# Performance work log

Measured on AMD Instinct MI355X. Metric: run time of the kernel, lower is better.

Reference implementation:

```python
import jax, jax.numpy as jnp
import numpy as np

B, T, H = 2, 2048, 1024
NH = 16
HD = H // NH


def setup_inputs() -> dict:
    key = jax.random.key(0)
    ks = jax.random.split(key, 9)
    s = 0.02
    return {
        "x": jax.random.normal(ks[0], (B, T, H), dtype=jnp.float32),
        "attn_mask": jnp.ones((B, T), dtype=jnp.int32),
        "Wq": jax.random.normal(ks[1], (H, H), dtype=jnp.float32) * s,
        "bq": jnp.zeros((H,), dtype=jnp.float32),
        "Wk": jax.random.normal(ks[2], (H, H), dtype=jnp.float32) * s,
        "bk": jnp.zeros((H,), dtype=jnp.float32),
        "Wv": jax.random.normal(ks[3], (H, H), dtype=jnp.float32) * s,
        "bv": jnp.zeros((H,), dtype=jnp.float32),
        "Wo": jax.random.normal(ks[4], (H, H), dtype=jnp.float32) * s,
        "bo": jnp.zeros((H,), dtype=jnp.float32),
    }


def reference(x, attn_mask, Wq, bq, Wk, bk, Wv, bv, Wo, bo):
    Bc, Tc, Hc = x.shape
    scale = HD ** -0.5
    # projections; torch Linear: y = x @ W.T + b (here W stored as [in,out])
    q = (x @ Wq + bq).reshape(Bc, Tc, NH, HD).transpose(0, 2, 1, 3)  # [B,NH,T,HD]
    k = (x @ Wk + bk).reshape(Bc, Tc, NH, HD).transpose(0, 2, 1, 3)
    v = (x @ Wv + bv).reshape(Bc, Tc, NH, HD).transpose(0, 2, 1, 3)
    scores = jnp.einsum('bhqd,bhkd->bhqk', q, k) * scale  # [B,NH,T,T]
    mask = attn_mask.reshape(Bc, 1, 1, Tc)
    scores = jnp.where(mask == 0, jnp.float32(-jnp.inf), scores)
    probs = jax.nn.softmax(scores, axis=-1)
    ctx = jnp.einsum('bhqk,bhkd->bhqd', probs, v)  # [B,NH,T,HD]
    ctx = ctx.transpose(0, 2, 1, 3).reshape(Bc, Tc, Hc)
    out = ctx @ Wo + bo
    return out
```

## Files before the change

### kernel.cpp

```cpp
#include <hip/hip_runtime.h>

typedef _Float16 f16;
typedef _Float16 f16x8 __attribute__((ext_vector_type(8)));
typedef _Float16 f16x4 __attribute__((ext_vector_type(4)));
typedef __fp16 h16x2 __attribute__((ext_vector_type(2)));
typedef float f32x4 __attribute__((ext_vector_type(4)));

#define MFMA32(a, b, c) __builtin_amdgcn_mfma_f32_16x16x32_f16((a), (b), (c), 0, 0, 0)
#define MFMA16(a, b, c) __builtin_amdgcn_mfma_f32_16x16x16f16((a), (b), (c), 0, 0, 0)

static constexpr int Bb = 2, T = 2048, H = 1024, NH = 16, HD = 64;
static constexpr int M = Bb * T;
static constexpr int NQKV = 3 * H;
#define QSCALE 0.1803368801111f

__device__ __forceinline__ void gload_lds16(const void* g, void* l) {
  __builtin_amdgcn_global_load_lds(
      (const __attribute__((address_space(1))) void*)g,
      (__attribute__((address_space(3))) void*)l, 16, 0, 0);
}


__global__ __launch_bounds__(256) void cvt_f32_f16_x4(const float* __restrict__ in,
                                                      f16* __restrict__ out, int n4) {
  int i = blockIdx.x * 256 + threadIdx.x;
  if (i < n4) {
    float4 v = ((const float4*)in)[i];
    f16x4 o;
    o[0] = (f16)v.x; o[1] = (f16)v.y; o[2] = (f16)v.z; o[3] = (f16)v.w;
    *(f16x4*)(out + (size_t)i * 4) = o;
  }
}

__global__ __launch_bounds__(256) void transpose_cvt4(const float* __restrict__ Wq,
                                                      const float* __restrict__ Wk,
                                                      const float* __restrict__ Wv,
                                                      const float* __restrict__ Wo,
                                                      f16* __restrict__ WqkvT,
                                                      f16* __restrict__ WoT) {
  const int z = blockIdx.z;
  const float* W = (z == 0) ? Wq : (z == 1) ? Wk : (z == 2) ? Wv : Wo;
  f16* Wt = (z < 3) ? (WqkvT + (size_t)z * H * H) : WoT;
  const float scale = (z == 0) ? QSCALE : 1.0f;
  __shared__ f16 tile[64][65];
  int k0 = blockIdx.y * 64, n0 = blockIdx.x * 64;
  for (int p = 0; p < 16; ++p) {
    int idx = threadIdx.x + p * 256;
    int r = idx >> 6, c = idx & 63;
    tile[r][c] = (f16)(W[(size_t)(k0 + r) * H + n0 + c] * scale);
  }
  __syncthreads();
  for (int p = 0; p < 16; ++p) {
    int idx = threadIdx.x + p * 256;
    int r = idx >> 6, c = idx & 63;
    Wt[(size_t)(n0 + r) * H + k0 + c] = tile[c][r];
  }
}

__global__ void pack_bias(const float* __restrict__ bq, const float* __restrict__ bk,
                          const float* __restrict__ bv, float* __restrict__ o) {
  int i = blockIdx.x * 256 + threadIdx.x;
  if (i < 3072) {
    float v = (i < 1024) ? bq[i] * QSCALE : ((i < 2048) ? bk[i - 1024] : bv[i - 2048]);
    o[i] = v;
  }
}

__device__ __forceinline__ f16x8 lds_frag(const f16* base, int row, int gr) {
  return *(const f16x8*)(base + row * 64 + ((gr ^ (row & 7)) << 3));
}

template <int TM, int TN, bool OUT_F32>
__global__ __launch_bounds__(256) void gemm_f16_bt(const f16* __restrict__ A,
                                                   const f16* __restrict__ Bt,
                                                   const float* __restrict__ bias,
                                                   void* __restrict__ Cout,
                                                   int Nn, int Kk) {
  __shared__ f16 As[TM * 64];
  __shared__ f16 Bs[TN * 64];
  const int tid = threadIdx.x;
  const int lane = tid & 63, w = tid >> 6;
  const int quad = lane >> 4, l16 = lane & 15;
  const int wm = w >> 1, wn = w & 1;
  const int m0 = blockIdx.y * TM, n0 = blockIdx.x * TN;
  constexpr int AM = TM / 32, AN = TN / 32;

  f32x4 acc[AM][AN];
  for (int a = 0; a < AM; ++a)
    for (int b2 = 0; b2 < AN; ++b2)
      for (int r = 0; r < 4; ++r) acc[a][b2][r] = 0.f;

  for (int k0 = 0; k0 < Kk; k0 += 64) {
    for (int p = 0; p < TM * 8 / 256; ++p) {
      int slot = p * 256 + w * 64 + lane;
      int r = slot >> 3, g = (slot & 7) ^ (r & 7);
      gload_lds16(A + (size_t)(m0 + r) * Kk + k0 + g * 8,
                  (char*)As + (p * 256 + w * 64) * 16);
    }
    for (int p = 0; p < TN * 8 / 256; ++p) {
      int slot = p * 256 + w * 64 + lane;
      int r = slot >> 3, g = (slot & 7) ^ (r & 7);
      gload_lds16(Bt + (size_t)(n0 + r) * Kk + k0 + g * 8,
                  (char*)Bs + (p * 256 + w * 64) * 16);
    }
    __syncthreads();
    for (int ks = 0; ks < 2; ++ks) {
      f16x8 af[AM], bf[AN];
      for (int t = 0; t < AM; ++t)
        af[t] = lds_frag(As, wm * (TM / 2) + t * 16 + l16, ks * 4 + quad);
      for (int t = 0; t < AN; ++t)
        bf[t] = lds_frag(Bs, wn * (TN / 2) + t * 16 + l16, ks * 4 + quad);
      for (int tm = 0; tm < AM; ++tm)
        for (int tn = 0; tn < AN; ++tn)
          acc[tm][tn] = MFMA32(af[tm], bf[tn], acc[tm][tn]);
    }
    __syncthreads();
  }

  for (int tm = 0; tm < AM; ++tm)
    for (int tn = 0; tn < AN; ++tn)
      for (int r = 0; r < 4; ++r) {
        int m = m0 + wm * (TM / 2) + tm * 16 + quad * 4 + r;
        int n = n0 + wn * (TN / 2) + tn * 16 + l16;
        float v = acc[tm][tn][r] + bias[n];
        if (OUT_F32)
          ((float*)Cout)[(size_t)m * Nn + n] = v;
        else
          ((f16*)Cout)[(size_t)m * Nn + n] = (f16)v;
      }
}


__global__ __launch_bounds__(256) void attn_fused(const f16* __restrict__ QKV,
                                                  const int* __restrict__ mask,
                                                  f16* __restrict__ ctx) {
  __shared__ f16 Kt[128 * 64];
  __shared__ f16 Vt[80 * 128];

  const int tid = threadIdx.x;
  const int w = tid >> 6, lane = tid & 63;
  const int quad = lane >> 4, l16 = lane & 15;
  const int q0 = blockIdx.x * 128, h = blockIdx.y, b = blockIdx.z;

  f16x8 qf[2][2];
  for (int tq = 0; tq < 2; ++tq) {
    const f16* qrow = QKV + (size_t)(b * T + q0 + w * 32 + tq * 16 + l16) * NQKV + h * HD;
    qf[tq][0] = *(const f16x8*)(qrow + quad * 8);
    qf[tq][1] = *(const f16x8*)(qrow + 32 + quad * 8);
  }

  f32x4 oacc[2][5];
  for (int tq = 0; tq < 2; ++tq)
    for (int t = 0; t < 5; ++t)
      for (int r = 0; r < 4; ++r) oacc[tq][t][r] = 0.f;

  const int vkv = tid & 127;
  const int vgb = (tid >> 7) * 4;

  for (int kv0 = 0; kv0 < T; kv0 += 128) {
    __syncthreads();
    for (int p = 0; p < 4; ++p) {
      int slot = p * 256 + w * 64 + lane;
      int r = slot >> 3, g = (slot & 7) ^ (r & 7);
      gload_lds16(QKV + (size_t)(b * T + kv0 + r) * NQKV + H + h * HD + g * 8,
                  (char*)Kt + (p * 256 + w * 64) * 16);
    }
    {
      f16 vm = (f16)(float)(mask[b * T + kv0 + vkv] != 0);
      const f16* vrow = QKV + (size_t)(b * T + kv0 + vkv) * NQKV + 2 * H + h * HD;
      for (int p = 0; p < 4; ++p) {
        int g = vgb + p;
        f16x8 v = *(const f16x8*)(vrow + g * 8);
        for (int j = 0; j < 8; ++j) {
          int d = g * 8 + j;
          Vt[d * 128 + ((vkv + 4 * (d & 15)) & 127)] = v[j] * vm;
        }
      }
      if (tid < 128) Vt[64 * 128 + vkv] = vm;
    }
    __syncthreads();

    for (int tk = 0; tk < 8; ++tk) {
      f16x8 kf0 = lds_frag(Kt, tk * 16 + l16, quad);
      f16x8 kf1 = lds_frag(Kt, tk * 16 + l16, 4 + quad);
      f16x4 vf[5];
      for (int td = 0; td < 5; ++td)
        vf[td] = *(const f16x4*)&Vt[(td * 16 + l16) * 128 +
                                    ((tk * 16 + quad * 4 + 4 * l16) & 127)];
      for (int tq = 0; tq < 2; ++tq) {
        f32x4 s = {0.f, 0.f, 0.f, 0.f};
        s = MFMA32(kf0, qf[tq][0], s);
        s = MFMA32(kf1, qf[tq][1], s);
        h16x2 p01 = __builtin_amdgcn_cvt_pkrtz(__builtin_amdgcn_exp2f(s[0]),
                                               __builtin_amdgcn_exp2f(s[1]));
        h16x2 p23 = __builtin_amdgcn_cvt_pkrtz(__builtin_amdgcn_exp2f(s[2]),
                                               __builtin_amdgcn_exp2f(s[3]));
        f16x4 pf;
        pf[0] = (f16)p01[0]; pf[1] = (f16)p01[1];
        pf[2] = (f16)p23[0]; pf[3] = (f16)p23[1];
        for (int td = 0; td < 5; ++td)
          oacc[tq][td] = MFMA16(vf[td], pf, oacc[tq][td]);
      }
    }
  }

  for (int tq = 0; tq < 2; ++tq) {
    float lq = __shfl(oacc[tq][4][0], l16, 64);
    float inv = 1.f / lq;
    int row = b * T + q0 + w * 32 + tq * 16 + l16;
    for (int td = 0; td < 4; ++td) {
      f16x4 o;
      for (int r = 0; r < 4; ++r) o[r] = (f16)(oacc[tq][td][r] * inv);
      *(f16x4*)(ctx + (size_t)row * H + h * HD + td * 16 + quad * 4) = o;
    }
  }
}


extern "C" void kernel_launch(void* const* d_in, const int* in_sizes, int n_in,
                              void* d_out, int out_size, void* d_ws, size_t ws_size,
                              hipStream_t stream) {
  const float* x  = (const float*)d_in[0];
  const int* mask = (const int*)d_in[1];
  const float* Wq = (const float*)d_in[2];
  const float* bq = (const float*)d_in[3];
  const float* Wk = (const float*)d_in[4];
  const float* bk = (const float*)d_in[5];
  const float* Wv = (const float*)d_in[6];
  const float* bv = (const float*)d_in[7];
  const float* Wo = (const float*)d_in[8];
  const float* bo = (const float*)d_in[9];
  float* out = (float*)d_out;

  char* ws = (char*)d_ws;
  f16* xh      = (f16*)(ws);
  f16* Wqkv_t  = (f16*)(ws + (8u  << 20));
  f16* Wot     = (f16*)(ws + (14u << 20));
  float* bqkv  = (float*)(ws + (16u << 20));
  f16* QKV     = (f16*)(ws + (17u << 20));
  f16* ctx     = (f16*)(ws + (42u << 20));

  cvt_f32_f16_x4<<<dim3((M * H / 4 + 255) / 256), 256, 0, stream>>>(x, xh, M * H / 4);
  transpose_cvt4<<<dim3(16, 16, 4), 256, 0, stream>>>(Wq, Wk, Wv, Wo, Wqkv_t, Wot);
  pack_bias<<<dim3(12), 256, 0, stream>>>(bq, bk, bv, bqkv);

  gemm_f16_bt<128, 128, false><<<dim3(NQKV / 128, M / 128), 256, 0, stream>>>(
      xh, Wqkv_t, bqkv, QKV, NQKV, H);

  attn_fused<<<dim3(T / 128, NH, Bb), 256, 0, stream>>>(QKV, mask, ctx);

  gemm_f16_bt<128, 64, true><<<dim3(H / 64, M / 128), 256, 0, stream>>>(
      ctx, Wot, bo, out, H, H);
}
```

Before: 223.6 us.

## Double-buffer K/V tiles in attention and merge prep kernels into one launch

The attention kernel now keeps two LDS buffers for K and V. It prefetches the next tile (K via async global-to-LDS, V into registers) while computing on the current one, which removes one barrier per iteration and hides load latency. Separately, the three preprocessing kernels (x conversion, weight transpose, bias pack) are merged into a single launch to cut launch overhead. The cost is doubled LDS use (about 73KB per block), which may lower occupancy, and extra registers for the V prefetch.

```diff
diff --git a/kernel.cpp b/kernel.cpp
--- a/kernel.cpp
+++ b/kernel.cpp
@@ -20,49 +20,50 @@
       (__attribute__((address_space(3))) void*)l, 16, 0, 0);
 }
 
-
-__global__ __launch_bounds__(256) void cvt_f32_f16_x4(const float* __restrict__ in,
-                                                      f16* __restrict__ out, int n4) {
-  int i = blockIdx.x * 256 + threadIdx.x;
-  if (i < n4) {
-    float4 v = ((const float4*)in)[i];
+__global__ __launch_bounds__(256) void pack_all(const float* __restrict__ x,
+                                                const float* __restrict__ Wq,
+                                                const float* __restrict__ Wk,
+                                                const float* __restrict__ Wv,
+                                                const float* __restrict__ Wo,
+                                                const float* __restrict__ bq,
+                                                const float* __restrict__ bk,
+                                                const float* __restrict__ bv,
+                                                f16* __restrict__ xh,
+                                                f16* __restrict__ WqkvT,
+                                                f16* __restrict__ WoT,
+                                                float* __restrict__ bqkv) {
+  __shared__ f16 tile[64][65];
+  const int bid = blockIdx.x;
+  if (bid < 4096) {
+    int i = bid * 256 + threadIdx.x;
+    float4 v = ((const float4*)x)[i];
     f16x4 o;
     o[0] = (f16)v.x; o[1] = (f16)v.y; o[2] = (f16)v.z; o[3] = (f16)v.w;
-    *(f16x4*)(out + (size_t)i * 4) = o;
-  }
-}
-
-__global__ __launch_bounds__(256) void transpose_cvt4(const float* __restrict__ Wq,
-                                                      const float* __restrict__ Wk,
-                                                      const float* __restrict__ Wv,
-                                                      const float* __restrict__ Wo,
-                                                      f16* __restrict__ WqkvT,
-                                                      f16* __restrict__ WoT) {
-  const int z = blockIdx.z;
-  const float* W = (z == 0) ? Wq : (z == 1) ? Wk : (z == 2) ? Wv : Wo;
-  f16* Wt = (z < 3) ? (WqkvT + (size_t)z * H * H) : WoT;
-  const float scale = (z == 0) ? QSCALE : 1.0f;
-  __shared__ f16 tile[64][65];
-  int k0 = blockIdx.y * 64, n0 = blockIdx.x * 64;
-  for (int p = 0; p < 16; ++p) {
-    int idx = threadIdx.x + p * 256;
-    int r = idx >> 6, c = idx & 63;
-    tile[r][c] = (f16)(W[(size_t)(k0 + r) * H + n0 + c] * scale);
-  }
-  __syncthreads();
-  for (int p = 0; p < 16; ++p) {
-    int idx = threadIdx.x + p * 256;
-    int r = idx >> 6, c = idx & 63;
-    Wt[(size_t)(n0 + r) * H + k0 + c] = tile[c][r];
-  }
-}
-
-__global__ void pack_bias(const float* __restrict__ bq, const float* __restrict__ bk,
-                          const float* __restrict__ bv, float* __restrict__ o) {
-  int i = blockIdx.x * 256 + threadIdx.x;
-  if (i < 3072) {
-    float v = (i < 1024) ? bq[i] * QSCALE : ((i < 2048) ? bk[i - 1024] : bv[i - 2048]);
-    o[i] = v;
+    *(f16x4*)(xh + (size_t)i * 4) = o;
+  } else if (bid < 5120) {
+    int t = bid - 4096;
+    int z = t >> 8, rem = t & 255;
+    const float* W = (z == 0) ? Wq : (z == 1) ? Wk : (z == 2) ? Wv : Wo;
+    f16* Wt = (z < 3) ? (WqkvT + (size_t)z * H * H) : WoT;
+    const float scale = (z == 0) ? QSCALE : 1.0f;
+    int k0 = (rem >> 4) * 64, n0 = (rem & 15) * 64;
+    for (int p = 0; p < 16; ++p) {
+      int idx = threadIdx.x + p * 256;
+      int r = idx >> 6, c = idx & 63;
+      tile[r][c] = (f16)(W[(size_t)(k0 + r) * H + n0 + c] * scale);
+    }
+    __syncthreads();
+    for (int p = 0; p < 16; ++p) {
+      int idx = threadIdx.x + p * 256;
+      int r = idx >> 6, c = idx & 63;
+      Wt[(size_t)(n0 + r) * H + k0 + c] = tile[c][r];
+    }
+  } else {
+    int i = (bid - 5120) * 256 + threadIdx.x;
+    if (i < 3072) {
+      float v = (i < 1024) ? bq[i] * QSCALE : ((i < 2048) ? bk[i - 1024] : bv[i - 2048]);
+      bqkv[i] = v;
+    }
   }
 }
 
@@ -134,13 +135,18 @@
 __global__ __launch_bounds__(256) void attn_fused(const f16* __restrict__ QKV,
                                                   const int* __restrict__ mask,
                                                   f16* __restrict__ ctx) {
-  __shared__ f16 Kt[128 * 64];
-  __shared__ f16 Vt[80 * 128];
+  __shared__ f16 Kt[2][128 * 64];
+  __shared__ f16 Vt[2][80 * 128];
 
   const int tid = threadIdx.x;
   const int w = tid >> 6, lane = tid & 63;
   const int quad = lane >> 4, l16 = lane & 15;
   const int q0 = blockIdx.x * 128, h = blockIdx.y, b = blockIdx.z;
+
+  const int vkv = tid & 127;
+  const int vgb = (tid >> 7) * 4;
+  const size_t kbase = (size_t)(b * T) * NQKV + H + h * HD;
+  const size_t vbase = (size_t)(b * T) * NQKV + 2 * H + h * HD;
 
   f16x8 qf[2][2];
   for (int tq = 0; tq < 2; ++tq) {
@@ -154,38 +160,55 @@
     for (int t = 0; t < 5; ++t)
       for (int r = 0; r < 4; ++r) oacc[tq][t][r] = 0.f;
 
-  const int vkv = tid & 127;
-  const int vgb = (tid >> 7) * 4;
-
-  for (int kv0 = 0; kv0 < T; kv0 += 128) {
-    __syncthreads();
+  for (int p = 0; p < 4; ++p) {
+    int slot = p * 256 + w * 64 + lane;
+    int r = slot >> 3, g = (slot & 7) ^ (r & 7);
+    gload_lds16(QKV + kbase + (size_t)r * NQKV + g * 8,
+                (char*)&Kt[0][0] + (p * 256 + w * 64) * 16);
+  }
+  {
+    f16 vm = (f16)(float)(mask[b * T + vkv] != 0);
+    const f16* vrow = QKV + vbase + (size_t)vkv * NQKV;
     for (int p = 0; p < 4; ++p) {
-      int slot = p * 256 + w * 64 + lane;
-      int r = slot >> 3, g = (slot & 7) ^ (r & 7);
-      gload_lds16(QKV + (size_t)(b * T + kv0 + r) * NQKV + H + h * HD + g * 8,
-                  (char*)Kt + (p * 256 + w * 64) * 16);
-    }
-    {
-      f16 vm = (f16)(float)(mask[b * T + kv0 + vkv] != 0);
-      const f16* vrow = QKV + (size_t)(b * T + kv0 + vkv) * NQKV + 2 * H + h * HD;
+      int g = vgb + p;
+      f16x8 v = *(const f16x8*)(vrow + g * 8);
+      for (int j = 0; j < 8; ++j) {
+        int d = g * 8 + j;
+        Vt[0][d * 128 + ((vkv + 4 * (d & 15)) & 127)] = v[j] * vm;
+      }
+    }
+    if (tid < 128) Vt[0][64 * 128 + vkv] = vm;
+  }
+  __syncthreads();
+
+  for (int it = 0; it < T / 128; ++it) {
+    const int cur = it & 1, nxt = cur ^ 1;
+    const int kvn = (it + 1) * 128;
+    const bool pf = kvn < T;
+
+    f16x8 vreg[4] = {};
+    f16 vm = (f16)0;
+    if (pf) {
       for (int p = 0; p < 4; ++p) {
-        int g = vgb + p;
-        f16x8 v = *(const f16x8*)(vrow + g * 8);
-        for (int j = 0; j < 8; ++j) {
-          int d = g * 8 + j;
-          Vt[d * 128 + ((vkv + 4 * (d & 15)) & 127)] = v[j] * vm;
-        }
-      }
-      if (tid < 128) Vt[64 * 128 + vkv] = vm;
-    }
-    __syncthreads();
-
+        int slot = p * 256 + w * 64 + lane;
+        int r = slot >> 3, g = (slot & 7) ^ (r & 7);
+        gload_lds16(QKV + kbase + (size_t)(kvn + r) * NQKV + g * 8,
+                    (char*)&Kt[nxt][0] + (p * 256 + w * 64) * 16);
+      }
+      vm = (f16)(float)(mask[b * T + kvn + vkv] != 0);
+      const f16* vrow = QKV + vbase + (size_t)(kvn + vkv) * NQKV;
+      for (int p = 0; p < 4; ++p)
+        vreg[p] = *(const f16x8*)(vrow + (vgb + p) * 8);
+    }
+
+    const f16* Kc = &Kt[cur][0];
+    const f16* Vc = &Vt[cur][0];
     for (int tk = 0; tk < 8; ++tk) {
-      f16x8 kf0 = lds_frag(Kt, tk * 16 + l16, quad);
-      f16x8 kf1 = lds_frag(Kt, tk * 16 + l16, 4 + quad);
+      f16x8 kf0 = lds_frag(Kc, tk * 16 + l16, quad);
+      f16x8 kf1 = lds_frag(Kc, tk * 16 + l16, 4 + quad);
       f16x4 vf[5];
       for (int td = 0; td < 5; ++td)
-        vf[td] = *(const f16x4*)&Vt[(td * 16 + l16) * 128 +
+        vf[td] = *(const f16x4*)&Vc[(td * 16 + l16) * 128 +
                                     ((tk * 16 + quad * 4 + 4 * l16) & 127)];
       for (int tq = 0; tq < 2; ++tq) {
         f32x4 s = {0.f, 0.f, 0.f, 0.f};
@@ -195,12 +218,24 @@
                                                __builtin_amdgcn_exp2f(s[1]));
         h16x2 p23 = __builtin_amdgcn_cvt_pkrtz(__builtin_amdgcn_exp2f(s[2]),
                                                __builtin_amdgcn_exp2f(s[3]));
-        f16x4 pf;
-        pf[0] = (f16)p01[0]; pf[1] = (f16)p01[1];
-        pf[2] = (f16)p23[0]; pf[3] = (f16)p23[1];
+        f16x4 pfr;
+        pfr[0] = (f16)p01[0]; pfr[1] = (f16)p01[1];
+        pfr[2] = (f16)p23[0]; pfr[3] = (f16)p23[1];
         for (int td = 0; td < 5; ++td)
-          oacc[tq][td] = MFMA16(vf[td], pf, oacc[tq][td]);
-      }
+          oacc[tq][td] = MFMA16(vf[td], pfr, oacc[tq][td]);
+      }
+    }
+
+    if (pf) {
+      for (int p = 0; p < 4; ++p) {
+        int g = vgb + p;
+        for (int j = 0; j < 8; ++j) {
+          int d = g * 8 + j;
+          Vt[nxt][d * 128 + (((kvn + vkv) + 4 * (d & 15)) & 127)] = vreg[p][j] * vm;
+        }
+      }
+      if (tid < 128) Vt[nxt][64 * 128 + vkv] = vm;
+      __syncthreads();
     }
   }
 
@@ -240,9 +275,8 @@
   f16* QKV     = (f16*)(ws + (17u << 20));
   f16* ctx     = (f16*)(ws + (42u << 20));
 
-  cvt_f32_f16_x4<<<dim3((M * H / 4 + 255) / 256), 256, 0, stream>>>(x, xh, M * H / 4);
-  transpose_cvt4<<<dim3(16, 16, 4), 256, 0, stream>>>(Wq, Wk, Wv, Wo, Wqkv_t, Wot);
-  pack_bias<<<dim3(12), 256, 0, stream>>>(bq, bk, bv, bqkv);
+  pack_all<<<dim3(5132), 256, 0, stream>>>(x, Wq, Wk, Wv, Wo, bq, bk, bv,
+                                           xh, Wqkv_t, Wot, bqkv);
 
   gemm_f16_bt<128, 128, false><<<dim3(NQKV / 128, M / 128), 256, 0, stream>>>(
       xh, Wqkv_t, bqkv, QKV, NQKV, H);
```

After: 212.1 us. -5.1%, faster.
